# Optimization experiments

Hardware: AMD Instinct MI355X
Metric: run time of the kernel (lower is better)

Reference implementation:

```python
import jax, jax.numpy as jnp
import numpy as np

B, T, D, H = 64, 1024, 1024, 1024


def setup_inputs() -> dict:
    key = jax.random.key(0)
    k = jax.random.split(key, 5)
    s = 1.0 / np.sqrt(H)  # torch RNNCell init: U(-1/sqrt(H), 1/sqrt(H))
    return {
        "x": jax.random.normal(k[0], (B, T, D), jnp.float32),
        "W_ih": jax.random.uniform(k[1], (H, D), jnp.float32, -s, s),
        "W_hh": jax.random.uniform(k[2], (H, H), jnp.float32, -s, s),
        "b_ih": jax.random.uniform(k[3], (H,), jnp.float32, -s, s),
        "b_hh": jax.random.uniform(k[4], (H,), jnp.float32, -s, s),
    }


def reference(x, W_ih, W_hh, b_ih, b_hh):
    # DelayLineRNN2xOS with a tanh RNNCell:
    #   for i in range(T//2):
    #     h_eve = cell(x[:, 2i],   h_eve); states[:, 2i]   = h_eve
    #     h_odd = cell(x[:, 2i-1], h_odd); states[:, 2i-1] = h_odd   (note 2*0-1 == -1)
    Bn, Tn, _ = x.shape
    Hn = W_hh.shape[0]
    half = Tn // 2

    idx_eve = jnp.arange(half) * 2          # 0, 2, ..., T-2
    idx_odd = (idx_eve - 1) % Tn            # T-1, 1, 3, ..., T-3  (Python neg-index at i=0)

    # Precompute input projections for all timesteps (both biases folded in).
    gi = jnp.einsum('btd,hd->bth', x, W_ih) + b_ih + b_hh  # [B, T, H]
    ge = gi[:, idx_eve].transpose(1, 0, 2)                  # [half, B, H]
    go = gi[:, idx_odd].transpose(1, 0, 2)                  # [half, B, H]

    h0 = jnp.zeros((Bn, Hn), x.dtype)

    def step(carry, inp):
        he, ho = carry
        a, b = inp
        he = jnp.tanh(a + he @ W_hh.T)
        ho = jnp.tanh(b + ho @ W_hh.T)
        return (he, ho), (he, ho)

    (he_f, ho_f), (eve_s, odd_s) = jax.lax.scan(step, (h0, h0), (ge, go))

    # eve_s[i] -> slot 2i ; odd_s[i] -> slot (2i-1) mod T, i.e. sorted odd slots
    # [1, 3, ..., T-1] receive odd_s rolled left by one.
    odd_sorted = jnp.roll(odd_s, -1, axis=0)                # [half, B, H]
    states = jnp.stack([eve_s, odd_sorted], axis=1)         # [half, 2, B, H]
    states = states.reshape(Tn, Bn, Hn).transpose(1, 0, 2)  # [B, T, H]

    return states, he_f[None]  # (states, h_final[1, B, H])
```

## Files before the change

### kernel.cpp

```cpp
#include <hip/hip_runtime.h>

#define B_    64
#define T_    1024
#define H_    1024
#define HALF_ 512
#define NWG_SCAN 128
#define HBUF_HALF 131072

typedef short bf16x8 __attribute__((ext_vector_type(8)));
typedef short bf16x4 __attribute__((ext_vector_type(4)));
typedef _Float16 f16x8 __attribute__((ext_vector_type(8)));
typedef float f32x4  __attribute__((ext_vector_type(4)));
typedef unsigned int u32x4 __attribute__((ext_vector_type(4)));
typedef unsigned int u32x2 __attribute__((ext_vector_type(2)));

__device__ __forceinline__ short f2h(float f) {
    return (short)__builtin_bit_cast(unsigned short, (_Float16)f);
}

__device__ __forceinline__ bf16x4 pk4(f32x4 v) {
    unsigned w0, w1;
    asm("v_cvt_pk_bf16_f32 %0, %1, %2" : "=v"(w0) : "v"(v.x), "v"(v.y));
    asm("v_cvt_pk_bf16_f32 %0, %1, %2" : "=v"(w1) : "v"(v.z), "v"(v.w));
    u32x2 r; r[0] = w0; r[1] = w1;
    return __builtin_bit_cast(bf16x4, r);
}

__device__ __forceinline__ float tanh_fast(float x) {
    return 1.0f - 2.0f / (__expf(2.0f * x) + 1.0f);
}

#define BAR() do { \
    __builtin_amdgcn_sched_barrier(0); \
    asm volatile("s_waitcnt lgkmcnt(0)" ::: "memory"); \
    __builtin_amdgcn_sched_barrier(0); \
    __builtin_amdgcn_s_barrier(); \
    __builtin_amdgcn_sched_barrier(0); \
} while (0)

__global__ __launch_bounds__(256) void gi_gemm(
        const float* __restrict__ X, const float* __restrict__ Wih,
        const float* __restrict__ bih, const float* __restrict__ bhh,
        float* __restrict__ out) {
    __shared__ short As[128][40];
    __shared__ short Bs[128][40];
    const int bid = blockIdx.x;
    const int tn = bid & 7;
    const int tm = bid >> 3;
    const int tid = threadIdx.x;
    const int l  = tid & 63;
    const int w  = tid >> 6;
    const int wr = w >> 1, wc = w & 1;
    const int lc = l & 15,  lr = l >> 4;

    const float* Ab = X   + (size_t)tm * 128 * 1024;
    const float* Bb = Wih + (size_t)tn * 128 * 1024;
    const int srow = tid >> 3;
    const int sc4  = (tid & 7) * 4;

    f32x4 acc[4][4];
#pragma unroll
    for (int m = 0; m < 4; m++)
#pragma unroll
        for (int n = 0; n < 4; n++) acc[m][n] = (f32x4){0.f, 0.f, 0.f, 0.f};

    f32x4 ra[4], rb[4];
#pragma unroll
    for (int c = 0; c < 4; c++) {
        ra[c] = *reinterpret_cast<const f32x4*>(Ab + (size_t)(srow + 32*c) * 1024 + sc4);
        rb[c] = *reinterpret_cast<const f32x4*>(Bb + (size_t)(srow + 32*c) * 1024 + sc4);
    }

    for (int k0 = 0; k0 < 1024; k0 += 32) {
        __syncthreads();
#pragma unroll
        for (int c = 0; c < 4; c++) {
            *reinterpret_cast<bf16x4*>(&As[srow + 32*c][sc4]) = pk4(ra[c]);
            *reinterpret_cast<bf16x4*>(&Bs[srow + 32*c][sc4]) = pk4(rb[c]);
        }
        __syncthreads();
        if (k0 + 32 < 1024) {
            const float* Ak = Ab + k0 + 32;
            const float* Bk = Bb + k0 + 32;
#pragma unroll
            for (int c = 0; c < 4; c++) {
                ra[c] = *reinterpret_cast<const f32x4*>(Ak + (size_t)(srow + 32*c) * 1024 + sc4);
                rb[c] = *reinterpret_cast<const f32x4*>(Bk + (size_t)(srow + 32*c) * 1024 + sc4);
            }
        }
        bf16x8 af[4], bfr[4];
#pragma unroll
        for (int m = 0; m < 4; m++)
            af[m] = *reinterpret_cast<bf16x8*>(&As[wr*64 + m*16 + lc][lr*8]);
#pragma unroll
        for (int n = 0; n < 4; n++)
            bfr[n] = *reinterpret_cast<bf16x8*>(&Bs[wc*64 + n*16 + lc][lr*8]);
#pragma unroll
        for (int m = 0; m < 4; m++)
#pragma unroll
            for (int n = 0; n < 4; n++)
                acc[m][n] = __builtin_amdgcn_mfma_f32_16x16x32_bf16(af[m], bfr[n], acc[m][n], 0, 0, 0);
    }

#pragma unroll
    for (int n = 0; n < 4; n++) {
        const int col = tn*128 + wc*64 + n*16 + lc;
        const float bs = bih[col] + bhh[col];
#pragma unroll
        for (int m = 0; m < 4; m++) {
            const int row0 = tm*128 + wr*64 + m*16 + lr*4;
#pragma unroll
            for (int j = 0; j < 4; j++)
                out[(size_t)(row0 + j) * 1024 + col] = acc[m][n][j] + bs;
        }
    }
}

__global__ __launch_bounds__(256, 1) void rnn_scan(
        const float* __restrict__ Whh, float* __restrict__ out,
        short* __restrict__ hbuf) {
    __shared__ short hB[16 * 1024];
    const int wg = blockIdx.x;
    const int p  = wg >> 6;
    const int g  = (wg >> 4) & 3;
    const int s  = wg & 15;
    const int tid = threadIdx.x;
    const int l  = tid & 63;
    const int w  = tid >> 6;
    const int lc = l & 15, lr = l >> 4;
    const int sb = tid >> 4;
    const int sg = tid & 15;

    bf16x8 breg[32];
    {
        const float* wrow = Whh + (size_t)(s*64 + w*16 + lc) * 1024;
#pragma unroll
        for (int kc = 0; kc < 32; kc++) {
            f32x4 v0 = *reinterpret_cast<const f32x4*>(wrow + kc*32 + lr*8);
            f32x4 v1 = *reinterpret_cast<const f32x4*>(wrow + kc*32 + lr*8 + 4);
            bf16x8 q = { f2h(v0.x), f2h(v0.y), f2h(v0.z), f2h(v0.w),
                         f2h(v1.x), f2h(v1.y), f2h(v1.z), f2h(v1.w) };
            breg[kc] = q;
        }
    }

    const unsigned hload_base = (unsigned)((p*64 + g*16 + sb) * 1024 + sg*8);
    const int batch = lc;
    const int col0  = s*64 + w*16 + lr*4;
    const unsigned hst_base = (unsigned)((p*64 + g*16 + batch) * 1024 + col0);

    int dly = 8;

    for (int step = 0; step < HALF_; step++) {
        const int tt = (p == 0) ? (2*step) : (step == 0 ? T_-1 : 2*step - 1);
        const int epw = step % 3 + 1;
        const int epv = (step + 2) % 3 + 1;
        f32x4 acc = (f32x4){0.f, 0.f, 0.f, 0.f};
        f32x4 giv;
        const unsigned ob = (unsigned)(((g*16 + batch) * T_ + tt) * H_ + col0);

        if (step) {
            for (int i = 0; i < dly; i++)
                asm volatile("s_sleep 1" ::: "memory");
            bf16x8 hl[8];
            const short* hc = hbuf + (size_t)((step+1) & 1) * HBUF_HALF + hload_base;
#pragma unroll
            for (int c = 0; c < 8; c++)
                asm volatile("global_load_dwordx4 %0, %1, off sc0 sc1"
                             : "=v"(hl[c]) : "v"(hc + c*128) : "memory");
            {
                const float* ga = out + ob;
                asm volatile("global_load_dwordx4 %0, %1, off"
                             : "=v"(giv) : "v"(ga) : "memory");
            }
            const unsigned pat = (unsigned)((epv & 1) | (((epv >> 1) & 1) << 16));
            unsigned pend = 0;
            asm volatile("s_waitcnt vmcnt(1)" ::: "memory");
            __builtin_amdgcn_sched_barrier(0);
#pragma unroll
            for (int c = 0; c < 8; c++) {
                u32x4 d = __builtin_bit_cast(u32x4, hl[c]);
                unsigned m = ((d[0] & 0x00010001u) ^ pat) | ((d[1] & 0x00010001u) ^ pat)
                           | ((d[2] & 0x00010001u) ^ pat) | ((d[3] & 0x00010001u) ^ pat);
                if (!__all(m == 0)) pend |= 1u << c;
            }
            const int hadRetry = (pend != 0);
            while (pend) {
#pragma unroll
                for (int c = 0; c < 8; c++)
                    if (pend & (1u << c))
                        asm volatile("global_load_dwordx4 %0, %1, off sc0 sc1"
                                     : "=v"(hl[c]) : "v"(hc + c*128) : "memory");
                asm volatile("s_waitcnt vmcnt(0)" ::: "memory");
                __builtin_amdgcn_sched_barrier(0);
#pragma unroll
                for (int c = 0; c < 8; c++) {
                    if (pend & (1u << c)) {
                        u32x4 d = __builtin_bit_cast(u32x4, hl[c]);
                        unsigned m = ((d[0] & 0x00010001u) ^ pat) | ((d[1] & 0x00010001u) ^ pat)
                                   | ((d[2] & 0x00010001u) ^ pat) | ((d[3] & 0x00010001u) ^ pat);
                        if (__all(m == 0)) pend &= ~(1u << c);
                    }
                }
            }
            dly = hadRetry ? (dly > 44 ? 48 : dly + 4) : (dly ? dly - 1 : 0);
#pragma unroll
            for (int c = 0; c < 8; c++) {
                bf16x4 lo = { hl[c][0], hl[c][1], hl[c][2], hl[c][3] };
                bf16x4 hi = { hl[c][4], hl[c][5], hl[c][6], hl[c][7] };
                const int g8 = (sg + c*16) * 2;
                *reinterpret_cast<bf16x4*>(&hB[sb*1024 + (((g8    ) ^ sb) << 2)]) = lo;
                *reinterpret_cast<bf16x4*>(&hB[sb*1024 + (((g8 + 1) ^ sb) << 2)]) = hi;
            }
            BAR();
            f32x4 a0 = (f32x4){0,0,0,0}, a1 = (f32x4){0,0,0,0};
            f32x4 a2 = (f32x4){0,0,0,0}, a3 = (f32x4){0,0,0,0};
#pragma unroll
            for (int kc = 0; kc < 32; kc += 4) {
#pragma unroll
                for (int q = 0; q < 4; q++) {
                    const int k8 = (kc + q) * 8 + lr * 2;
                    bf16x4 lo = *reinterpret_cast<const bf16x4*>(&hB[lc*1024 + (((k8    ) ^ lc) << 2)]);
                    bf16x4 hi = *reinterpret_cast<const bf16x4*>(&hB[lc*1024 + (((k8 + 1) ^ lc) << 2)]);
                    bf16x8 hf = { lo[0], lo[1], lo[2], lo[3], hi[0], hi[1], hi[2], hi[3] };
                    f32x4& aq = (q == 0) ? a0 : (q == 1) ? a1 : (q == 2) ? a2 : a3;
                    aq = __builtin_amdgcn_mfma_f32_16x16x32_f16(
                        __builtin_bit_cast(f16x8, breg[kc + q]),
                        __builtin_bit_cast(f16x8, hf), aq, 0, 0, 0);
                }
            }
            acc = (a0 + a1) + (a2 + a3);
        } else {
            const float* ga = out + ob;
            asm volatile("global_load_dwordx4 %0, %1, off"
                         : "=v"(giv) : "v"(ga) : "memory");
        }

        asm volatile("s_waitcnt vmcnt(0)" ::: "memory");
        __builtin_amdgcn_sched_barrier(0);

        float hv0 = tanh_fast(acc[0] + giv[0]);
        float hv1 = tanh_fast(acc[1] + giv[1]);
        float hv2 = tanh_fast(acc[2] + giv[2]);
        float hv3 = tanh_fast(acc[3] + giv[3]);
        const unsigned e0 = (unsigned)(epw & 1);
        const unsigned e1 = (unsigned)((epw >> 1) & 1);
        unsigned u0 = ((unsigned)__builtin_bit_cast(unsigned short, (_Float16)hv0) & 0xFFFEu) | e0;
        unsigned u1 = ((unsigned)__builtin_bit_cast(unsigned short, (_Float16)hv1) & 0xFFFEu) | e1;
        unsigned u2 = ((unsigned)__builtin_bit_cast(unsigned short, (_Float16)hv2) & 0xFFFEu) | e0;
        unsigned u3 = ((unsigned)__builtin_bit_cast(unsigned short, (_Float16)hv3) & 0xFFFEu) | e1;
        u32x2 pk; pk[0] = u0 | (u1 << 16); pk[1] = u2 | (u3 << 16);

        if (step < HALF_ - 1) {
            short* hn = hbuf + (size_t)(step & 1) * HBUF_HALF + hst_base;
            asm volatile("global_store_dwordx2 %0, %1, off sc0 sc1"
                         :: "v"(hn), "v"(pk) : "memory");
        }

        {
            f32x4 ov; ov[0] = hv0; ov[1] = hv1; ov[2] = hv2; ov[3] = hv3;
            float* op_ = out + ob;
            asm volatile("global_store_dwordx4 %0, %1, off"
                         :: "v"(op_), "v"(ov) : "memory");
            if (p == 0 && step == HALF_ - 1) {
                float* fp_ = out + (size_t)B_*T_*H_ + (size_t)((g*16 + batch) * H_ + col0);
                asm volatile("global_store_dwordx4 %0, %1, off"
                             :: "v"(fp_), "v"(ov) : "memory");
            }
        }

        BAR();
    }
}

extern "C" void kernel_launch(void* const* d_in, const int* in_sizes, int n_in,
                              void* d_out, int out_size, void* d_ws, size_t ws_size,
                              hipStream_t stream) {
    const float* X   = (const float*)d_in[0];
    const float* Wih = (const float*)d_in[1];
    const float* Whh = (const float*)d_in[2];
    const float* bih = (const float*)d_in[3];
    const float* bhh = (const float*)d_in[4];
    float* out = (float*)d_out;

    short* hbuf = (short*)d_ws;

    hipMemsetAsync(hbuf, 0, (size_t)2 * HBUF_HALF * 2, stream);
    gi_gemm<<<dim3(4096), dim3(256), 0, stream>>>(X, Wih, bih, bhh, out);
    rnn_scan<<<dim3(NWG_SCAN), dim3(256), 0, stream>>>(Whh, out, hbuf);
}
```

Measured before the change: 1.955 ms.

## Transpose gi loads and state stores through LDS; change hbuf to MFMA-fragment layout

The gi load and the output-state store now go through LDS staging buffers. Each 16-lane group therefore touches a contiguous 256-byte row segment instead of scattered 16-byte pieces per batch row. The hbuf exchange layout now follows the MFMA output fragment order, so each thread stores and loads contiguous chunks, and the LDS scatter is recomputed to match. This aims to cut memory-transaction overhead on the latency-critical per-step path. In exchange it adds LDS round trips, an extra barrier on step 0 and a full vmcnt wait before the LDS writes.

```diff
diff --git a/kernel.cpp b/kernel.cpp
--- a/kernel.cpp
+++ b/kernel.cpp
@@ -120,6 +120,8 @@
         const float* __restrict__ Whh, float* __restrict__ out,
         short* __restrict__ hbuf) {
     __shared__ short hB[16 * 1024];
+    __shared__ float giS[16 * 68];
+    __shared__ float htrF[16 * 68];
     const int wg = blockIdx.x;
     const int p  = wg >> 6;
     const int g  = (wg >> 4) & 3;
@@ -144,10 +146,9 @@
         }
     }
 
-    const unsigned hload_base = (unsigned)((p*64 + g*16 + sb) * 1024 + sg*8);
-    const int batch = lc;
-    const int col0  = s*64 + w*16 + lr*4;
-    const unsigned hst_base = (unsigned)((p*64 + g*16 + batch) * 1024 + col0);
+    const unsigned grp_base = (unsigned)((p*64 + g*16) * 1024);
+    const unsigned hst_off = grp_base + (unsigned)(s*1024 + w*256 + lr*64 + lc*4);
+    const int lcol = w*16 + lr*4;
 
     int dly = 8;
 
@@ -157,22 +158,20 @@
         const int epv = (step + 2) % 3 + 1;
         f32x4 acc = (f32x4){0.f, 0.f, 0.f, 0.f};
         f32x4 giv;
-        const unsigned ob = (unsigned)(((g*16 + batch) * T_ + tt) * H_ + col0);
+        const float* ga = out + (size_t)(((g*16 + sb) * T_ + tt) * H_ + s*64 + sg*4);
 
         if (step) {
             for (int i = 0; i < dly; i++)
                 asm volatile("s_sleep 1" ::: "memory");
             bf16x8 hl[8];
-            const short* hc = hbuf + (size_t)((step+1) & 1) * HBUF_HALF + hload_base;
+            const short* hc = hbuf + (size_t)((step+1) & 1) * HBUF_HALF
+                            + grp_base + (unsigned)(tid*8);
 #pragma unroll
             for (int c = 0; c < 8; c++)
                 asm volatile("global_load_dwordx4 %0, %1, off sc0 sc1"
-                             : "=v"(hl[c]) : "v"(hc + c*128) : "memory");
-            {
-                const float* ga = out + ob;
-                asm volatile("global_load_dwordx4 %0, %1, off"
-                             : "=v"(giv) : "v"(ga) : "memory");
-            }
+                             : "=v"(hl[c]) : "v"(hc + c*2048) : "memory");
+            asm volatile("global_load_dwordx4 %0, %1, off"
+                         : "=v"(giv) : "v"(ga) : "memory");
             const unsigned pat = (unsigned)((epv & 1) | (((epv >> 1) & 1) << 16));
             unsigned pend = 0;
             asm volatile("s_waitcnt vmcnt(1)" ::: "memory");
@@ -190,7 +189,7 @@
                 for (int c = 0; c < 8; c++)
                     if (pend & (1u << c))
                         asm volatile("global_load_dwordx4 %0, %1, off sc0 sc1"
-                                     : "=v"(hl[c]) : "v"(hc + c*128) : "memory");
+                                     : "=v"(hl[c]) : "v"(hc + c*2048) : "memory");
                 asm volatile("s_waitcnt vmcnt(0)" ::: "memory");
                 __builtin_amdgcn_sched_barrier(0);
 #pragma unroll
@@ -204,13 +203,18 @@
                 }
             }
             dly = hadRetry ? (dly > 44 ? 48 : dly + 4) : (dly ? dly - 1 : 0);
+            asm volatile("s_waitcnt vmcnt(0)" ::: "memory");
+            __builtin_amdgcn_sched_barrier(0);
+            *reinterpret_cast<f32x4*>(&giS[sb*68 + sg*4]) = giv;
 #pragma unroll
             for (int c = 0; c < 8; c++) {
                 bf16x4 lo = { hl[c][0], hl[c][1], hl[c][2], hl[c][3] };
                 bf16x4 hi = { hl[c][4], hl[c][5], hl[c][6], hl[c][7] };
-                const int g8 = (sg + c*16) * 2;
-                *reinterpret_cast<bf16x4*>(&hB[sb*1024 + (((g8    ) ^ sb) << 2)]) = lo;
-                *reinterpret_cast<bf16x4*>(&hB[sb*1024 + (((g8 + 1) ^ sb) << 2)]) = hi;
+                const int gidx0 = c*512 + tid*2;
+                const int b0 = gidx0 & 15;
+                const int g8 = gidx0 >> 4;
+                *reinterpret_cast<bf16x4*>(&hB[b0*1024 + ((g8 ^ b0) << 2)]) = lo;
+                *reinterpret_cast<bf16x4*>(&hB[(b0+1)*1024 + ((g8 ^ (b0+1)) << 2)]) = hi;
             }
             BAR();
             f32x4 a0 = (f32x4){0,0,0,0}, a1 = (f32x4){0,0,0,0};
@@ -231,18 +235,20 @@
             }
             acc = (a0 + a1) + (a2 + a3);
         } else {
-            const float* ga = out + ob;
             asm volatile("global_load_dwordx4 %0, %1, off"
                          : "=v"(giv) : "v"(ga) : "memory");
-        }
-
-        asm volatile("s_waitcnt vmcnt(0)" ::: "memory");
-        __builtin_amdgcn_sched_barrier(0);
-
-        float hv0 = tanh_fast(acc[0] + giv[0]);
-        float hv1 = tanh_fast(acc[1] + giv[1]);
-        float hv2 = tanh_fast(acc[2] + giv[2]);
-        float hv3 = tanh_fast(acc[3] + giv[3]);
+            asm volatile("s_waitcnt vmcnt(0)" ::: "memory");
+            __builtin_amdgcn_sched_barrier(0);
+            *reinterpret_cast<f32x4*>(&giS[sb*68 + sg*4]) = giv;
+            BAR();
+        }
+
+        f32x4 gi4 = *reinterpret_cast<f32x4*>(&giS[lc*68 + lcol]);
+
+        float hv0 = tanh_fast(acc[0] + gi4[0]);
+        float hv1 = tanh_fast(acc[1] + gi4[1]);
+        float hv2 = tanh_fast(acc[2] + gi4[2]);
+        float hv3 = tanh_fast(acc[3] + gi4[3]);
         const unsigned e0 = (unsigned)(epw & 1);
         const unsigned e1 = (unsigned)((epw >> 1) & 1);
         unsigned u0 = ((unsigned)__builtin_bit_cast(unsigned short, (_Float16)hv0) & 0xFFFEu) | e0;
@@ -252,24 +258,27 @@
         u32x2 pk; pk[0] = u0 | (u1 << 16); pk[1] = u2 | (u3 << 16);
 
         if (step < HALF_ - 1) {
-            short* hn = hbuf + (size_t)(step & 1) * HBUF_HALF + hst_base;
+            short* hn = hbuf + (size_t)(step & 1) * HBUF_HALF + hst_off;
             asm volatile("global_store_dwordx2 %0, %1, off sc0 sc1"
                          :: "v"(hn), "v"(pk) : "memory");
         }
 
         {
-            f32x4 ov; ov[0] = hv0; ov[1] = hv1; ov[2] = hv2; ov[3] = hv3;
-            float* op_ = out + ob;
+            f32x4 hv; hv[0] = hv0; hv[1] = hv1; hv[2] = hv2; hv[3] = hv3;
+            *reinterpret_cast<f32x4*>(&htrF[lc*68 + lcol]) = hv;
+        }
+        BAR();
+        {
+            f32x4 ov = *reinterpret_cast<f32x4*>(&htrF[sb*68 + sg*4]);
+            float* op_ = out + (size_t)(((g*16 + sb) * T_ + tt) * H_ + s*64 + sg*4);
             asm volatile("global_store_dwordx4 %0, %1, off"
                          :: "v"(op_), "v"(ov) : "memory");
             if (p == 0 && step == HALF_ - 1) {
-                float* fp_ = out + (size_t)B_*T_*H_ + (size_t)((g*16 + batch) * H_ + col0);
+                float* fp_ = out + (size_t)B_*T_*H_ + (size_t)((g*16 + sb) * H_ + s*64 + sg*4);
                 asm volatile("global_store_dwordx4 %0, %1, off"
                              :: "v"(fp_), "v"(ov) : "memory");
             }
         }
-
-        BAR();
     }
 }
 
```

Result: faster. 1.790 ms, median of 2 (-8.4%).
